# Optimization experiments

Measured on AMD Instinct MI355X. Metric: run time of the kernel, lower is better.

The kernel has to match this reference:

```python
import jax, jax.numpy as jnp
import numpy as np

B, N, C = 8, 1024, 768
H = 12
HD = C // H
STAGES = 3
MLP_H = 4 * C
EPS = 1e-5


def _layernorm(x, w, b):
    mu = jnp.mean(x, axis=-1, keepdims=True)
    var = jnp.mean(jnp.square(x - mu), axis=-1, keepdims=True)
    return (x - mu) * jax.lax.rsqrt(var + EPS) * w + b


def setup_inputs() -> dict:
    key = jax.random.key(0)
    ks = jax.random.split(key, 16)
    s = 0.02
    return {
        "x": jax.random.normal(ks[0], (B, N, C), dtype=jnp.float32),
        # stacked per-stage attention params (torch Linear layout: [out, in])
        "qkv_w": jax.random.normal(ks[1], (STAGES, 3 * C, C), dtype=jnp.float32) * s,
        "proj_w": jax.random.normal(ks[2], (STAGES, C, C), dtype=jnp.float32) * s,
        "proj_b": jnp.zeros((STAGES, C), dtype=jnp.float32),
        "ln1_w": jnp.ones((C,), dtype=jnp.float32),
        "ln1_b": jnp.zeros((C,), dtype=jnp.float32),
        "ln2_w": jnp.ones((C,), dtype=jnp.float32),
        "ln2_b": jnp.zeros((C,), dtype=jnp.float32),
        "mlp_w1": jax.random.normal(ks[3], (MLP_H, C), dtype=jnp.float32) * s,
        "mlp_b1": jnp.zeros((MLP_H,), dtype=jnp.float32),
        "mlp_w2": jax.random.normal(ks[4], (C, MLP_H), dtype=jnp.float32) * s,
        "mlp_b2": jnp.zeros((C,), dtype=jnp.float32),
        "focus_w": jnp.ones((STAGES,), dtype=jnp.float32),
    }


def reference(x, qkv_w, proj_w, proj_b, ln1_w, ln1_b, ln2_w, ln2_b,
              mlp_w1, mlp_b1, mlp_w2, mlp_b2, focus_w):
    scale = HD ** -0.5
    h = _layernorm(x, ln1_w, ln1_b)  # shared norm1(x) input to all stages
    attn_out = jnp.zeros_like(x)
    for i in range(STAGES):
        qkv = jnp.einsum('bnc,oc->bno', h, qkv_w[i])  # [B,N,3C], no bias (qkv_bias=False)
        qkv = qkv.reshape(B, N, 3, H, HD).transpose(2, 0, 3, 1, 4)  # [3,B,H,N,HD]
        q, k, v = qkv[0], qkv[1], qkv[2]
        attn = jax.nn.softmax(jnp.einsum('bhnd,bhmd->bhnm', q, k) * scale, axis=-1)
        o = jnp.einsum('bhnm,bhmd->bhnd', attn, v)  # [B,H,N,HD]
        o = o.transpose(0, 2, 1, 3).reshape(B, N, C)
        o = jnp.einsum('bnc,oc->bno', o, proj_w[i]) + proj_b[i]
        attn_out = attn_out + focus_w[i] * o
    x = x + attn_out
    h2 = _layernorm(x, ln2_w, ln2_b)
    h2 = jax.nn.gelu(jnp.einsum('bnc,hc->bnh', h2, mlp_w1) + mlp_b1, approximate=False)
    mlp_out = jnp.einsum('bnh,ch->bnc', h2, mlp_w2) + mlp_b2
    return x + mlp_out
```

## Files before the change

### kernel.cpp

```cpp
#include <hip/hip_runtime.h>
#include <hip/hip_bf16.h>
#include <math.h>

#define B_    8
#define N_    1024
#define C_    768
#define H_    12
#define HD_   64
#define MLPH_ 3072
#define M_ROWS 8192
#define QKV3  6912
#define PK    2304

typedef float  f32x4   __attribute__((ext_vector_type(4)));
typedef float  f32x16  __attribute__((ext_vector_type(16)));
typedef __bf16 bf16x8  __attribute__((ext_vector_type(8)));

__device__ __forceinline__ f32x4 mfma16(bf16x8 a, bf16x8 b, f32x4 c) {
    return __builtin_amdgcn_mfma_f32_16x16x32_bf16(a, b, c, 0, 0, 0);
}
__device__ __forceinline__ f32x16 mfma32(bf16x8 a, bf16x8 b, f32x16 c) {
    return __builtin_amdgcn_mfma_f32_32x32x16_bf16(a, b, c, 0, 0, 0);
}

__device__ __forceinline__ void gl16(const __bf16* g, __bf16* l) {
    __builtin_amdgcn_global_load_lds(
        (const __attribute__((address_space(1))) unsigned int*)g,
        (__attribute__((address_space(3))) unsigned int*)l,
        16, 0, 0);
}

__device__ __forceinline__ unsigned packbf(float a, float b) {
    __bf16 x = (__bf16)a, y = (__bf16)b;
    union { __bf16 h; unsigned short u; } ux, uy;
    ux.h = x; uy.h = y;
    return (unsigned)ux.u | ((unsigned)uy.u << 16);
}

__global__ __launch_bounds__(256) void cast_f32_bf16(const float* __restrict__ in,
                                                     __bf16* __restrict__ out, int n) {
    int i = blockIdx.x * 256 + threadIdx.x;
    if (i < n) out[i] = (__bf16)in[i];
}

__global__ __launch_bounds__(256) void prep_proj_w(const float* __restrict__ pw,
                                                   const float* __restrict__ focus,
                                                   __bf16* __restrict__ out) {
    int i = blockIdx.x * 256 + threadIdx.x;
    int c = i % C_;
    int s = (i / C_) % 3;
    int o = i / PK;
    out[i] = (__bf16)(focus[s] * pw[((size_t)s * C_ + o) * C_ + c]);
}

__global__ __launch_bounds__(256) void ln_to_bf16(const float* __restrict__ x,
                                                  const float* __restrict__ g,
                                                  const float* __restrict__ bta,
                                                  __bf16* __restrict__ out) {
    int row = blockIdx.x;
    const float* xr = x + (size_t)row * C_;
    int t = threadIdx.x;
    float v0 = xr[t], v1 = xr[t + 256], v2 = xr[t + 512];
    float s  = v0 + v1 + v2;
    float s2 = v0 * v0 + v1 * v1 + v2 * v2;
#pragma unroll
    for (int m = 1; m < 64; m <<= 1) { s += __shfl_xor(s, m); s2 += __shfl_xor(s2, m); }
    __shared__ float red[8];
    int w = t >> 6, lane = t & 63;
    if (lane == 0) { red[w] = s; red[4 + w] = s2; }
    __syncthreads();
    s  = red[0] + red[1] + red[2] + red[3];
    s2 = red[4] + red[5] + red[6] + red[7];
    float mu   = s * (1.f / C_);
    float var  = s2 * (1.f / C_) - mu * mu;
    float rstd = rsqrtf(var + 1e-5f);
    __bf16* orow = out + (size_t)row * C_;
    orow[t]       = (__bf16)((v0 - mu) * rstd * g[t]       + bta[t]);
    orow[t + 256] = (__bf16)((v1 - mu) * rstd * g[t + 256] + bta[t + 256]);
    orow[t + 512] = (__bf16)((v2 - mu) * rstd * g[t + 512] + bta[t + 512]);
}

template <int MODE>
__global__ __launch_bounds__(256) void gemm_bt(
    const __bf16* __restrict__ A, const __bf16* __restrict__ W,
    int M, int N, int K,
    __bf16* __restrict__ obf, float* __restrict__ of32,
    const float* __restrict__ resid, const float* __restrict__ bias,
    const float* __restrict__ focus_p)
{
    __shared__ __bf16 As[3][128][32];
    __shared__ __bf16 Bs[3][128][32];

    const int t    = threadIdx.x;
    const int lane = t & 63;
    const int w    = t >> 6;
    const int wr   = w >> 1, wc = w & 1;
    const int m0   = blockIdx.y * 128, n0 = blockIdx.x * 128;
    const int lo   = lane & 15;

    const int srow = lane >> 2;
    const int scol = (((lane & 3) ^ ((lane >> 3) & 3))) * 8;
    const int rcol = ((((lane >> 4) & 3) ^ ((lane >> 1) & 3))) * 8;

    auto stage = [&](int buf, int k0) {
#pragma unroll
        for (int i = 0; i < 2; i++) {
            const int chunk = w * 2 + i;
            const int row   = chunk * 16 + srow;
            gl16(&A[(size_t)(m0 + row) * K + k0 + scol], &As[buf][chunk * 16][0]);
            gl16(&W[(size_t)(n0 + row) * K + k0 + scol], &Bs[buf][chunk * 16][0]);
        }
    };

    const int nT = K >> 5;
    stage(0, 0);
    stage(1, 32);
    stage(2, 64);

    f32x4 acc[4][4] = {};
    int cur = 0;
    for (int tt = 0; tt < nT; ++tt) {
        const int rem = nT - tt;
        if (rem > 2)       asm volatile("s_waitcnt vmcnt(8)" ::: "memory");
        else if (rem == 2) asm volatile("s_waitcnt vmcnt(4)" ::: "memory");
        else               asm volatile("s_waitcnt vmcnt(0)" ::: "memory");
        __builtin_amdgcn_s_barrier();
        __builtin_amdgcn_sched_barrier(0);

        bf16x8 af[4], bfr[4];
#pragma unroll
        for (int mi = 0; mi < 4; mi++) af[mi]  = *(const bf16x8*)&As[cur][wr * 64 + mi * 16 + lo][rcol];
#pragma unroll
        for (int ni = 0; ni < 4; ni++) bfr[ni] = *(const bf16x8*)&Bs[cur][wc * 64 + ni * 16 + lo][rcol];
#pragma unroll
        for (int mi = 0; mi < 4; mi++)
#pragma unroll
            for (int ni = 0; ni < 4; ni++)
                acc[mi][ni] = mfma16(af[mi], bfr[ni], acc[mi][ni]);

        asm volatile("s_waitcnt lgkmcnt(0)" ::: "memory");
        __builtin_amdgcn_s_barrier();
        if (tt + 3 < nT) stage(cur, (tt + 3) * 32);
        cur = (cur == 2) ? 0 : cur + 1;
    }

    float f0 = 0.f, f1 = 0.f, f2 = 0.f;
    if (MODE == 1) { f0 = focus_p[0]; f1 = focus_p[1]; f2 = focus_p[2]; }

#pragma unroll
    for (int mi = 0; mi < 4; mi++) {
#pragma unroll
        for (int ni = 0; ni < 4; ni++) {
            int col = n0 + wc * 64 + ni * 16 + lo;
#pragma unroll
            for (int r = 0; r < 4; r++) {
                int row = m0 + wr * 64 + mi * 16 + (lane >> 4) * 4 + r;
                size_t o = (size_t)row * N + col;
                float v = acc[mi][ni][r];
                if (MODE == 0) {
                    obf[o] = (__bf16)v;
                } else if (MODE == 1) {
                    float be = f0 * bias[col] + f1 * bias[col + C_] + f2 * bias[col + 2 * C_];
                    of32[o] = resid[o] + v + be;
                } else if (MODE == 2) {
                    float u = v + bias[col];
                    float ge = 0.5f * u * (1.0f + erff(u * 0.70710678118654752f));
                    obf[o] = (__bf16)ge;
                } else {
                    of32[o] = resid[o] + v + bias[col];
                }
            }
        }
    }
}

__global__ __launch_bounds__(256) void attn_kernel(const __bf16* __restrict__ qkv,
                                                   __bf16* __restrict__ obuf) {
    const int bid  = blockIdx.x;
    const int idx  = bid >> 3;
    const int grp  = (bid & 7) * 36 + (idx >> 3);
    const int qt   = idx & 7;
    const int s    = grp / 96;
    const int rem  = grp % 96;
    const int b    = rem / 12;
    const int h    = rem % 12;
    const int q0   = qt * 128;

    const int t = threadIdx.x, lane = t & 63, w = t >> 6;
    const int l31 = lane & 31, hi1 = lane >> 5;

    __shared__ __bf16 Kf[4096];
    __shared__ __bf16 Vf[4096];
    __shared__ float  Lsm[128];

    const size_t rs = QKV3;
    const __bf16* qb = qkv + (size_t)b * N_ * rs + (size_t)s * PK + h * HD_;
    const __bf16* kb = qb + C_;
    const __bf16* vb = qb + 2 * C_;

    const float cexp = 0.18033688011112042f;

    bf16x8 aq[4];
#pragma unroll
    for (int dk = 0; dk < 4; dk++) {
        aq[dk] = *(const bf16x8*)(qb + (size_t)(q0 + w * 32 + l31) * rs + dk * 16 + hi1 * 8);
#pragma unroll
        for (int j = 0; j < 8; j++) aq[dk][j] = (__bf16)((float)aq[dk][j] * cexp);
    }

    f32x16 oacc[2] = {};
    float lsum = 0.f;

    int4 kreg[2]; uint4 vreg[2];
    auto load_tile = [&](int k0) {
#pragma unroll
        for (int p = 0; p < 2; p++) {
            int id = p * 256 + t;
            int kr = id >> 3, d0 = (id & 7) * 8;
            kreg[p] = *(const int4*)(kb + (size_t)(k0 + kr) * rs + d0);
            int kr2 = id & 63, d2 = ((id >> 6) * 8);
            vreg[p] = *(const uint4*)(vb + (size_t)(k0 + kr2) * rs + d2);
        }
    };
    load_tile(0);

    for (int kt = 0; kt < 16; kt++) {
        __syncthreads();
#pragma unroll
        for (int p = 0; p < 2; p++) {
            int id = p * 256 + t;
            int chunk = (id & 7) * 64 + (id >> 3);
            int c = chunk ^ (id & 7);
            *(int4*)&Kf[c * 8] = kreg[p];
        }
        {
            int k8 = lane >> 3, par = lane & 1, koff = lane & 6;
#pragma unroll
            for (int p = 0; p < 2; p++) {
                int d2 = ((p * 256 + t) >> 6) * 8;
#pragma unroll
                for (int i = 0; i < 4; i++) {
                    unsigned mw = vreg[p][i];
                    unsigned pw = (unsigned)__builtin_amdgcn_mov_dpp((int)mw, 0xB1, 0xF, 0xF, true);
                    unsigned out = par ? ((pw >> 16) | (mw & 0xFFFF0000u))
                                       : ((mw & 0xFFFFu) | (pw << 16));
                    int d = d2 + 2 * i + par;
                    int chunk = k8 * 64 + d;
                    int c = chunk ^ k8;
                    *(unsigned*)&Vf[c * 8 + koff] = out;
                }
            }
        }
        __syncthreads();
        if (kt < 15) load_tile((kt + 1) * 64);

        f32x16 sacc[2] = {};
#pragma unroll
        for (int ks = 0; ks < 2; ks++)
#pragma unroll
            for (int dk = 0; dk < 4; dk++) {
                int d8 = dk * 2 + hi1;
                int c = (d8 * 64 + ks * 32 + l31) ^ d8;
                bf16x8 kf = *(const bf16x8*)&Kf[c * 8];
                sacc[ks] = mfma32(kf, aq[dk], sacc[ks]);
            }

#pragma unroll
        for (int ks = 0; ks < 2; ks++) {
            float pe[16];
#pragma unroll
            for (int r = 0; r < 16; r++) {
                pe[r] = __builtin_amdgcn_exp2f(sacc[ks][r]);
                lsum += pe[r];
            }
            unsigned pk[8];
#pragma unroll
            for (int i = 0; i < 8; i++) pk[i] = packbf(pe[2 * i], pe[2 * i + 1]);

            unsigned a0 = pk[0], a2 = pk[2], a1 = pk[1], a3 = pk[3];
            {
                auto r0 = __builtin_amdgcn_permlane32_swap((int)a0, (int)a2, false, false);
                a0 = (unsigned)r0[0]; a2 = (unsigned)r0[1];
                auto r1 = __builtin_amdgcn_permlane32_swap((int)a1, (int)a3, false, false);
                a1 = (unsigned)r1[0]; a3 = (unsigned)r1[1];
            }
            unsigned b0 = pk[4], b2 = pk[6], b1 = pk[5], b3 = pk[7];
            {
                auto r0 = __builtin_amdgcn_permlane32_swap((int)b0, (int)b2, false, false);
                b0 = (unsigned)r0[0]; b2 = (unsigned)r0[1];
                auto r1 = __builtin_amdgcn_permlane32_swap((int)b1, (int)b3, false, false);
                b1 = (unsigned)r1[0]; b3 = (unsigned)r1[1];
            }
            union { unsigned u[4]; bf16x8 v; } fr0, fr1;
            fr0.u[0] = a0; fr0.u[1] = a1; fr0.u[2] = a2; fr0.u[3] = a3;
            fr1.u[0] = b0; fr1.u[1] = b1; fr1.u[2] = b2; fr1.u[3] = b3;

#pragma unroll
            for (int f = 0; f < 2; f++) {
                bf16x8 pa = f ? fr1.v : fr0.v;
#pragma unroll
                for (int dh = 0; dh < 2; dh++) {
                    int k8 = ks * 4 + f * 2 + hi1;
                    int c = (k8 * 64 + dh * 32 + l31) ^ k8;
                    bf16x8 vf = *(const bf16x8*)&Vf[c * 8];
                    oacc[dh] = mfma32(pa, vf, oacc[dh]);
                }
            }
        }
    }

    float ls2 = lsum + __shfl_xor(lsum, 32);
    if (lane < 32) Lsm[w * 32 + lane] = ls2;
    f32x4 Ls[4];
#pragma unroll
    for (int g = 0; g < 4; g++)
        Ls[g] = *(const f32x4*)&Lsm[w * 32 + 8 * g + 4 * hi1];

    __bf16* obase = obuf + ((size_t)b * N_ + q0 + w * 32) * PK + (size_t)s * C_ + h * HD_ + l31;
#pragma unroll
    for (int g = 0; g < 4; g++)
#pragma unroll
        for (int i = 0; i < 4; i++) {
            float inv = 1.0f / Ls[g][i];
            int q_local = i + 8 * g + 4 * hi1;
            __bf16* orow = obase + (size_t)q_local * PK;
            orow[0]  = (__bf16)(oacc[0][4 * g + i] * inv);
            orow[32] = (__bf16)(oacc[1][4 * g + i] * inv);
        }
}

extern "C" void kernel_launch(void* const* d_in, const int* in_sizes, int n_in,
                              void* d_out, int out_size, void* d_ws, size_t ws_size,
                              hipStream_t stream) {
    const float* x      = (const float*)d_in[0];
    const float* qkv_w  = (const float*)d_in[1];
    const float* proj_w = (const float*)d_in[2];
    const float* proj_b = (const float*)d_in[3];
    const float* ln1_w  = (const float*)d_in[4];
    const float* ln1_b  = (const float*)d_in[5];
    const float* ln2_w  = (const float*)d_in[6];
    const float* ln2_b  = (const float*)d_in[7];
    const float* mlp_w1 = (const float*)d_in[8];
    const float* mlp_b1 = (const float*)d_in[9];
    const float* mlp_w2 = (const float*)d_in[10];
    const float* mlp_b2 = (const float*)d_in[11];
    const float* focus  = (const float*)d_in[12];
    float* out = (float*)d_out;

    char* ws = (char*)d_ws;
    size_t off = 0;
    auto alloc = [&](size_t bytes) {
        char* p = ws + off;
        off += (bytes + 255) & ~(size_t)255;
        return p;
    };
    __bf16* h1   = (__bf16*)alloc((size_t)M_ROWS * C_ * 2);
    __bf16* qkvb = (__bf16*)alloc((size_t)M_ROWS * QKV3 * 2);
    __bf16* ob   = (__bf16*)alloc((size_t)M_ROWS * PK * 2);
    float*  x1   = (float*) alloc((size_t)M_ROWS * C_ * 4);
    __bf16* wq   = (__bf16*)alloc((size_t)QKV3 * C_ * 2);
    __bf16* wp   = (__bf16*)alloc((size_t)C_ * PK * 2);
    __bf16* w1   = (__bf16*)alloc((size_t)MLPH_ * C_ * 2);
    __bf16* w2   = (__bf16*)alloc((size_t)C_ * MLPH_ * 2);
    if (off > ws_size) return;
    __bf16* h2  = h1;
    __bf16* hid = qkvb;

    const int nq = QKV3 * C_;
    const int np = C_ * PK;
    const int n1 = MLPH_ * C_;
    cast_f32_bf16<<<(nq + 255) / 256, 256, 0, stream>>>(qkv_w, wq, nq);
    prep_proj_w<<<(np + 255) / 256, 256, 0, stream>>>(proj_w, focus, wp);
    cast_f32_bf16<<<(n1 + 255) / 256, 256, 0, stream>>>(mlp_w1, w1, n1);
    cast_f32_bf16<<<(n1 + 255) / 256, 256, 0, stream>>>(mlp_w2, w2, n1);

    ln_to_bf16<<<M_ROWS, 256, 0, stream>>>(x, ln1_w, ln1_b, h1);

    gemm_bt<0><<<dim3(QKV3 / 128, M_ROWS / 128), 256, 0, stream>>>(
        h1, wq, M_ROWS, QKV3, C_, qkvb, nullptr, nullptr, nullptr, nullptr);

    attn_kernel<<<3 * B_ * H_ * (N_ / 128), 256, 0, stream>>>(qkvb, ob);

    gemm_bt<1><<<dim3(C_ / 128, M_ROWS / 128), 256, 0, stream>>>(
        ob, wp, M_ROWS, C_, PK, nullptr, x1, x, proj_b, focus);

    ln_to_bf16<<<M_ROWS, 256, 0, stream>>>(x1, ln2_w, ln2_b, h2);

    gemm_bt<2><<<dim3(MLPH_ / 128, M_ROWS / 128), 256, 0, stream>>>(
        h2, w1, M_ROWS, MLPH_, C_, hid, nullptr, nullptr, mlp_b1, nullptr);
    gemm_bt<3><<<dim3(C_ / 128, M_ROWS / 128), 256, 0, stream>>>(
        hid, w2, M_ROWS, C_, MLPH_, nullptr, out, x1, mlp_b2, nullptr);
}
```

Before: 492.4 us.

## Add 256x256-tile 8-wave GEMM kernel for QKV and MLP up-projection

Adds a new GEMM kernel with 512 threads and 256x256 output tiles. It uses double-buffered LDS with an XOR swizzle, a remapped workgroup order so neighbouring blocks share tiles, and raised wave priority around the MFMA bursts. The QKV GEMM and the first MLP GEMM (with fused bias+GELU) now use this kernel instead of the 128x128 one, aiming for more data reuse per block and less global and LDS traffic. The larger tile raises register and LDS pressure, and the 32x27 tile grid may be uneven across CUs.

```diff
diff --git a/kernel.cpp b/kernel.cpp
--- a/kernel.cpp
+++ b/kernel.cpp
@@ -81,6 +81,96 @@
 }
 
 template <int MODE>
+__global__ __launch_bounds__(512, 2) void gemm8(
+    const __bf16* __restrict__ A, const __bf16* __restrict__ W,
+    int M, int N, int K, int ntn,
+    __bf16* __restrict__ obf, const float* __restrict__ bias)
+{
+    __shared__ __bf16 L[2][2][2][16][512];
+
+    const int t = threadIdx.x, lane = t & 63, w = t >> 6;
+    const int wm = w >> 2, wn = w & 3;
+    const int lo = lane & 15, hi = lane >> 4;
+
+    const int nwg = gridDim.x;
+    const int bid = blockIdx.x;
+    const int wgid = (bid & 7) * (nwg >> 3) + (bid >> 3);
+    const int m0 = (wgid / ntn) * 256, n0 = (wgid % ntn) * 256;
+
+    const int r16 = lane >> 2;
+    const int cc  = ((lane & 3) * 8) ^ ((lane >> 1) & 16);
+
+    auto stage = [&](int buf, int kh, int k0) {
+        __bf16* la = &L[buf][0][kh][2 * w][0];
+        const size_t ra = (size_t)(m0 + 2 * w * 16 + r16) * K + k0 + cc;
+        gl16(&A[ra], la);
+        gl16(&A[ra + (size_t)16 * K], la + 512);
+        __bf16* lb = &L[buf][1][kh][2 * w][0];
+        const size_t rb = (size_t)(n0 + 2 * w * 16 + r16) * K + k0 + cc;
+        gl16(&W[rb], lb);
+        gl16(&W[rb + (size_t)16 * K], lb + 512);
+    };
+
+    const int rdoff = lo * 32 + ((hi * 8) ^ ((lo << 1) & 16));
+
+    const int nkt = K >> 6;
+    stage(0, 0, 0);
+    stage(0, 1, 32);
+
+    f32x4 acc[8][4] = {};
+
+    for (int kt = 0; kt < nkt; ++kt) {
+        const int buf = kt & 1;
+#pragma unroll
+        for (int kh = 0; kh < 2; ++kh) {
+            if (kt == nkt - 1 && kh == 1) asm volatile("s_waitcnt vmcnt(0)" ::: "memory");
+            else                          asm volatile("s_waitcnt vmcnt(4)" ::: "memory");
+            __builtin_amdgcn_s_barrier();
+            __builtin_amdgcn_sched_barrier(0);
+            if (kt + 1 < nkt) stage(buf ^ 1, kh, (kt + 1) * 64 + kh * 32);
+
+            bf16x8 af[8], bfr[4];
+#pragma unroll
+            for (int mf = 0; mf < 8; mf++)
+                af[mf] = *(const bf16x8*)&L[buf][0][kh][wm * 8 + mf][rdoff];
+#pragma unroll
+            for (int nf = 0; nf < 4; nf++)
+                bfr[nf] = *(const bf16x8*)&L[buf][1][kh][wn * 4 + nf][rdoff];
+            asm volatile("s_waitcnt lgkmcnt(0)" ::: "memory");
+            __builtin_amdgcn_sched_barrier(0);
+            __builtin_amdgcn_s_setprio(1);
+#pragma unroll
+            for (int mf = 0; mf < 8; mf++)
+#pragma unroll
+                for (int nf = 0; nf < 4; nf++)
+                    acc[mf][nf] = mfma16(af[mf], bfr[nf], acc[mf][nf]);
+            __builtin_amdgcn_s_setprio(0);
+        }
+    }
+
+#pragma unroll
+    for (int mf = 0; mf < 8; mf++) {
+#pragma unroll
+        for (int nf = 0; nf < 4; nf++) {
+            const int col = n0 + wn * 64 + nf * 16 + lo;
+#pragma unroll
+            for (int r = 0; r < 4; r++) {
+                const int row = m0 + wm * 128 + mf * 16 + hi * 4 + r;
+                const size_t o = (size_t)row * N + col;
+                float v = acc[mf][nf][r];
+                if (MODE == 0) {
+                    obf[o] = (__bf16)v;
+                } else {
+                    float u = v + bias[col];
+                    float ge = 0.5f * u * (1.0f + erff(u * 0.70710678118654752f));
+                    obf[o] = (__bf16)ge;
+                }
+            }
+        }
+    }
+}
+
+template <int MODE>
 __global__ __launch_bounds__(256) void gemm_bt(
     const __bf16* __restrict__ A, const __bf16* __restrict__ W,
     int M, int N, int K,
@@ -157,15 +247,9 @@
                 int row = m0 + wr * 64 + mi * 16 + (lane >> 4) * 4 + r;
                 size_t o = (size_t)row * N + col;
                 float v = acc[mi][ni][r];
-                if (MODE == 0) {
-                    obf[o] = (__bf16)v;
-                } else if (MODE == 1) {
+                if (MODE == 1) {
                     float be = f0 * bias[col] + f1 * bias[col + C_] + f2 * bias[col + 2 * C_];
                     of32[o] = resid[o] + v + be;
-                } else if (MODE == 2) {
-                    float u = v + bias[col];
-                    float ge = 0.5f * u * (1.0f + erff(u * 0.70710678118654752f));
-                    obf[o] = (__bf16)ge;
                 } else {
                     of32[o] = resid[o] + v + bias[col];
                 }
@@ -376,8 +460,8 @@
 
     ln_to_bf16<<<M_ROWS, 256, 0, stream>>>(x, ln1_w, ln1_b, h1);
 
-    gemm_bt<0><<<dim3(QKV3 / 128, M_ROWS / 128), 256, 0, stream>>>(
-        h1, wq, M_ROWS, QKV3, C_, qkvb, nullptr, nullptr, nullptr, nullptr);
+    gemm8<0><<<(M_ROWS / 256) * (QKV3 / 256), 512, 0, stream>>>(
+        h1, wq, M_ROWS, QKV3, C_, QKV3 / 256, qkvb, nullptr);
 
     attn_kernel<<<3 * B_ * H_ * (N_ / 128), 256, 0, stream>>>(qkvb, ob);
 
@@ -386,8 +470,9 @@
 
     ln_to_bf16<<<M_ROWS, 256, 0, stream>>>(x1, ln2_w, ln2_b, h2);
 
-    gemm_bt<2><<<dim3(MLPH_ / 128, M_ROWS / 128), 256, 0, stream>>>(
-        h2, w1, M_ROWS, MLPH_, C_, hid, nullptr, nullptr, mlp_b1, nullptr);
+    gemm8<2><<<(M_ROWS / 256) * (MLPH_ / 256), 512, 0, stream>>>(
+        h2, w1, M_ROWS, MLPH_, C_, MLPH_ / 256, hid, mlp_b1);
+
     gemm_bt<3><<<dim3(C_ / 128, M_ROWS / 128), 256, 0, stream>>>(
         hid, w2, M_ROWS, C_, MLPH_, nullptr, out, x1, mlp_b2, nullptr);
 }
```

Result: no change. 490.3 us (-0.4%).
